# Optimization experiments

Hardware: AMD Instinct MI355X
Metric: run time of the kernel (lower is better)

Reference implementation:

```python
import jax, jax.numpy as jnp
import numpy as np

N = 131072
C = 1000

def setup_inputs() -> dict:
    key = jax.random.key(0)
    k1, k2 = jax.random.split(key)
    predicted = jax.random.normal(k1, (N, C), dtype=jnp.float32)
    # soft labels (need not sum to 1; original just uses target[:, y].float())
    target = jax.random.uniform(k2, (N, C), dtype=jnp.float32)
    return {"predicted": predicted, "target": target}

def reference(predicted, target):
    # Original loops over classes y, computing cross_entropy(predicted, y)
    # = -log_softmax(predicted)[:, y], weighted by target[:, y] and summed.
    # Fused form: per-row weighted sum of -log_softmax, then mean over rows.
    logp = jax.nn.log_softmax(predicted, axis=-1)          # [N, C]
    per_point = -jnp.sum(target * logp, axis=-1)           # [N]
    return jnp.mean(per_point)
```

## Files before the change

### kernel.cpp

```cpp
#include <hip/hip_runtime.h>


typedef float f32x4 __attribute__((ext_vector_type(4)));

#define WAVES_PER_BLOCK 4
#define BLOCK_THREADS 256
#define NBLOCKS 2048

__global__ __launch_bounds__(BLOCK_THREADS, 8)
void ce_rows_kernel(const float* __restrict__ pred,
                    const float* __restrict__ targ,
                    float* __restrict__ partial,
                    int nrows, int C) {
    const int lane = threadIdx.x & 63;
    const int wid  = threadIdx.x >> 6;
    const int waves_total = gridDim.x * WAVES_PER_BLOCK;
    const int wave_global = blockIdx.x * WAVES_PER_BLOCK + wid;
    const int C4 = C >> 2;

    float acc_lse = 0.0f;
    float acc_tp  = 0.0f;

    for (int row = wave_global; row < nrows; row += waves_total) {
        const f32x4* __restrict__ p4 = (const f32x4*)(pred + (size_t)row * C);
        const f32x4* __restrict__ t4 = (const f32x4*)(targ + (size_t)row * C);

        f32x4 pv[4];
        float m = -3.0e38f;
        #pragma unroll
        for (int it = 0; it < 4; ++it) {
            int idx = lane + it * 64;
            if (idx < C4) pv[it] = __builtin_nontemporal_load(p4 + idx);
        }
        #pragma unroll
        for (int it = 0; it < 4; ++it) {
            int idx = lane + it * 64;
            if (idx < C4)
                m = fmaxf(m, fmaxf(fmaxf(pv[it][0], pv[it][1]),
                                   fmaxf(pv[it][2], pv[it][3])));
        }
        #pragma unroll
        for (int off = 32; off > 0; off >>= 1)
            m = fmaxf(m, __shfl_xor(m, off, 64));

        float se = 0.0f, st = 0.0f;
        #pragma unroll
        for (int it = 0; it < 4; ++it) {
            int idx = lane + it * 64;
            if (idx < C4) {
                f32x4 t = __builtin_nontemporal_load(t4 + idx);
                f32x4 p = pv[it];
                se += __expf(p[0] - m) + __expf(p[1] - m)
                    + __expf(p[2] - m) + __expf(p[3] - m);
                st += (t[0] + t[1]) + (t[2] + t[3]);
                acc_tp += t[0]*p[0] + t[1]*p[1] + t[2]*p[2] + t[3]*p[3];
            }
        }
        #pragma unroll
        for (int off = 32; off > 0; off >>= 1) {
            se += __shfl_xor(se, off, 64);
            st += __shfl_xor(st, off, 64);
        }
        acc_lse += (m + __logf(se)) * st;
    }

    #pragma unroll
    for (int off = 32; off > 0; off >>= 1)
        acc_tp += __shfl_xor(acc_tp, off, 64);

    float wave_sum = acc_lse - acc_tp;

    __shared__ float lds[WAVES_PER_BLOCK];
    if (lane == 0) lds[wid] = wave_sum;
    __syncthreads();
    if (threadIdx.x == 0) {
        float s = 0.0f;
        #pragma unroll
        for (int i = 0; i < WAVES_PER_BLOCK; ++i) s += lds[i];
        partial[blockIdx.x] = s;
    }
}

__global__ __launch_bounds__(256)
void ce_reduce_kernel(const float* __restrict__ partial, int n,
                      float* __restrict__ out, float inv_n) {
    __shared__ float lds[256];
    float s = 0.0f;
    for (int i = threadIdx.x; i < n; i += 256) s += partial[i];
    lds[threadIdx.x] = s;
    __syncthreads();
    #pragma unroll
    for (int stride = 128; stride > 0; stride >>= 1) {
        if ((int)threadIdx.x < stride) lds[threadIdx.x] += lds[threadIdx.x + stride];
        __syncthreads();
    }
    if (threadIdx.x == 0) out[0] = lds[0] * inv_n;
}

extern "C" void kernel_launch(void* const* d_in, const int* in_sizes, int n_in,
                              void* d_out, int out_size, void* d_ws, size_t ws_size,
                              hipStream_t stream) {
    const float* pred = (const float*)d_in[0];
    const float* targ = (const float*)d_in[1];
    float* out = (float*)d_out;

    const int C = 1000;
    const int N = in_sizes[0] / C;

    int nblocks = NBLOCKS;
    if ((size_t)nblocks * sizeof(float) > ws_size)
        nblocks = (int)(ws_size / sizeof(float));
    if (nblocks < 1) nblocks = 1;

    float* partial = (float*)d_ws;

    ce_rows_kernel<<<nblocks, BLOCK_THREADS, 0, stream>>>(pred, targ, partial, N, C);
    ce_reduce_kernel<<<1, 256, 0, stream>>>(partial, nblocks, out, 1.0f / (float)N);
}
```

Before: 174.6 us.

## Fuse final reduction via last-block atomic counter and hoist target loads

```diff
diff --git a/kernel.cpp b/kernel.cpp
--- a/kernel.cpp
+++ b/kernel.cpp
@@ -8,10 +8,12 @@
 #define NBLOCKS 2048
 
 __global__ __launch_bounds__(BLOCK_THREADS, 8)
-void ce_rows_kernel(const float* __restrict__ pred,
-                    const float* __restrict__ targ,
-                    float* __restrict__ partial,
-                    int nrows, int C) {
+void ce_fused_kernel(const float* __restrict__ pred,
+                     const float* __restrict__ targ,
+                     float* __restrict__ partial,
+                     unsigned int* __restrict__ counter,
+                     float* __restrict__ out,
+                     int nrows, int C, float inv_n) {
     const int lane = threadIdx.x & 63;
     const int wid  = threadIdx.x >> 6;
     const int waves_total = gridDim.x * WAVES_PER_BLOCK;
@@ -25,13 +27,19 @@
         const f32x4* __restrict__ p4 = (const f32x4*)(pred + (size_t)row * C);
         const f32x4* __restrict__ t4 = (const f32x4*)(targ + (size_t)row * C);
 
-        f32x4 pv[4];
-        float m = -3.0e38f;
+        f32x4 pv[4], tv[4];
         #pragma unroll
         for (int it = 0; it < 4; ++it) {
             int idx = lane + it * 64;
             if (idx < C4) pv[it] = __builtin_nontemporal_load(p4 + idx);
         }
+        #pragma unroll
+        for (int it = 0; it < 4; ++it) {
+            int idx = lane + it * 64;
+            if (idx < C4) tv[it] = __builtin_nontemporal_load(t4 + idx);
+        }
+
+        float m = -3.0e38f;
         #pragma unroll
         for (int it = 0; it < 4; ++it) {
             int idx = lane + it * 64;
@@ -48,7 +56,7 @@
         for (int it = 0; it < 4; ++it) {
             int idx = lane + it * 64;
             if (idx < C4) {
-                f32x4 t = __builtin_nontemporal_load(t4 + idx);
+                f32x4 t = tv[it];
                 f32x4 p = pv[it];
                 se += __expf(p[0] - m) + __expf(p[1] - m)
                     + __expf(p[2] - m) + __expf(p[3] - m);
@@ -70,31 +78,35 @@
 
     float wave_sum = acc_lse - acc_tp;
 
-    __shared__ float lds[WAVES_PER_BLOCK];
-    if (lane == 0) lds[wid] = wave_sum;
+    __shared__ float wsum[WAVES_PER_BLOCK];
+    __shared__ float red[BLOCK_THREADS];
+    __shared__ int   is_last;
+    if (lane == 0) wsum[wid] = wave_sum;
     __syncthreads();
     if (threadIdx.x == 0) {
+        float s = wsum[0] + wsum[1] + wsum[2] + wsum[3];
+        partial[blockIdx.x] = s;
+        __threadfence();
+        unsigned int old = atomicAdd(counter, 1u);
+        is_last = (old == (unsigned int)(gridDim.x - 1)) ? 1 : 0;
+    }
+    __syncthreads();
+
+    if (is_last) {
+        __threadfence();
+        volatile const float* pv_part = (volatile const float*)partial;
         float s = 0.0f;
+        for (int i = threadIdx.x; i < (int)gridDim.x; i += BLOCK_THREADS)
+            s += pv_part[i];
+        red[threadIdx.x] = s;
+        __syncthreads();
         #pragma unroll
-        for (int i = 0; i < WAVES_PER_BLOCK; ++i) s += lds[i];
-        partial[blockIdx.x] = s;
+        for (int stride = BLOCK_THREADS / 2; stride > 0; stride >>= 1) {
+            if ((int)threadIdx.x < stride) red[threadIdx.x] += red[threadIdx.x + stride];
+            __syncthreads();
+        }
+        if (threadIdx.x == 0) out[0] = red[0] * inv_n;
     }
-}
-
-__global__ __launch_bounds__(256)
-void ce_reduce_kernel(const float* __restrict__ partial, int n,
-                      float* __restrict__ out, float inv_n) {
-    __shared__ float lds[256];
-    float s = 0.0f;
-    for (int i = threadIdx.x; i < n; i += 256) s += partial[i];
-    lds[threadIdx.x] = s;
-    __syncthreads();
-    #pragma unroll
-    for (int stride = 128; stride > 0; stride >>= 1) {
-        if ((int)threadIdx.x < stride) lds[threadIdx.x] += lds[threadIdx.x + stride];
-        __syncthreads();
-    }
-    if (threadIdx.x == 0) out[0] = lds[0] * inv_n;
 }
 
 extern "C" void kernel_launch(void* const* d_in, const int* in_sizes, int n_in,
@@ -107,13 +119,17 @@
     const int C = 1000;
     const int N = in_sizes[0] / C;
 
+    unsigned int* counter = (unsigned int*)d_ws;
+    float* partial = (float*)d_ws + 16;
+
     int nblocks = NBLOCKS;
-    if ((size_t)nblocks * sizeof(float) > ws_size)
-        nblocks = (int)(ws_size / sizeof(float));
+    size_t need = (size_t)(16 + nblocks) * sizeof(float);
+    if (need > ws_size)
+        nblocks = (int)(ws_size / sizeof(float)) - 16;
     if (nblocks < 1) nblocks = 1;
 
-    float* partial = (float*)d_ws;
+    hipMemsetAsync(counter, 0, sizeof(unsigned int), stream);
 
-    ce_rows_kernel<<<nblocks, BLOCK_THREADS, 0, stream>>>(pred, targ, partial, N, C);
-    ce_reduce_kernel<<<1, 256, 0, stream>>>(partial, nblocks, out, 1.0f / (float)N);
+    ce_fused_kernel<<<nblocks, BLOCK_THREADS, 0, stream>>>(
+        pred, targ, partial, counter, out, N, C, 1.0f / (float)N);
 }
```

Result: slower. 261.1 us (+49.6%).
